# Kernel tuning notes

Measured on AMD Instinct MI355X. Metric: run time of the kernel, lower is better.

The kernel has to match this reference:

```python
import jax, jax.numpy as jnp
import numpy as np

L = 2          # num_blocks
E = 256        # embed_features
FIN = 64       # input_features
FF = 4 * E     # dim_feedforward
OUT = 10       # out_dim
WCTX = 64      # context_len
B, S = 2, 1024
LN_EPS = 1e-5


def _ln(x, g, b):
    m = jnp.mean(x, axis=-1, keepdims=True)
    v = jnp.mean((x - m) ** 2, axis=-1, keepdims=True)
    return (x - m) / jnp.sqrt(v + LN_EPS) * g + b


def setup_inputs() -> dict:
    key = jax.random.key(0)
    ks = jax.random.split(key, 12)
    s = 0.02
    return {
        "inputs": jax.random.normal(ks[0], (B, S, FIN), jnp.float32),
        "embed_w": jax.random.normal(ks[1], (E, FIN), jnp.float32) * s,
        "embed_b": jnp.zeros((E,), jnp.float32),
        "qkv_w": jax.random.normal(ks[2], (L, 3 * E, E), jnp.float32) * s,
        "qkv_b": jnp.zeros((L, 3 * E), jnp.float32),
        "attn_out_w": jax.random.normal(ks[3], (L, E, E), jnp.float32) * s,
        "attn_out_b": jnp.zeros((L, E), jnp.float32),
        "ln1_g": jnp.ones((L, E), jnp.float32),
        "ln1_b": jnp.zeros((L, E), jnp.float32),
        "ffn1_w": jax.random.normal(ks[4], (L, FF, E), jnp.float32) * s,
        "ffn1_b": jnp.zeros((L, FF), jnp.float32),
        "ffn2_w": jax.random.normal(ks[5], (L, E, FF), jnp.float32) * s,
        "ffn2_b": jnp.zeros((L, E), jnp.float32),
        "ln2_g": jnp.ones((L, E), jnp.float32),
        "ln2_b": jnp.zeros((L, E), jnp.float32),
        "head_w": jax.random.normal(ks[6], (OUT, E), jnp.float32) * s,
        "head_b": jnp.zeros((OUT,), jnp.float32),
        "context_len": WCTX,
    }


def reference(inputs, embed_w, embed_b, qkv_w, qkv_b, attn_out_w, attn_out_b,
              ln1_g, ln1_b, ffn1_w, ffn1_b, ffn2_w, ffn2_b, ln2_g, ln2_b,
              head_w, head_b, context_len):
    b, s, _ = inputs.shape
    e = embed_w.shape[0]
    nh = max(1, e // 64) * 2           # torch: nhead = max(1, E//64)*2
    hd = e // nh
    scale = 1.0 / np.sqrt(hd)
    w = context_len

    emb = inputs @ embed_w.T + embed_b                       # [B,S,E]
    # left-pad with W-1 zeros so window pos p = padded[p:p+W] (zeros for early pos)
    padded = jnp.pad(emb, ((0, 0), (w - 1, 0), (0, 0)))
    idx = jnp.arange(s)[:, None] + jnp.arange(w)[None, :]    # [S,W]
    x = padded[:, idx].reshape(b * s, w, e)                  # [B*S,W,E]

    nlayers = qkv_w.shape[0]
    for l in range(nlayers):
        qkv = x @ qkv_w[l].T + qkv_b[l]                      # [N,W,3E]
        q, k, v = jnp.split(qkv, 3, axis=-1)
        q = q.reshape(-1, w, nh, hd)
        k = k.reshape(-1, w, nh, hd)
        v = v.reshape(-1, w, nh, hd)
        scores = jnp.einsum('nqhd,nkhd->nhqk', q, k) * scale
        attn = jax.nn.softmax(scores, axis=-1)
        o = jnp.einsum('nhqk,nkhd->nqhd', attn, v).reshape(-1, w, e)
        o = o @ attn_out_w[l].T + attn_out_b[l]
        x = _ln(x + o, ln1_g[l], ln1_b[l])                   # post-norm (torch default)
        ff = jax.nn.silu(x @ ffn1_w[l].T + ffn1_b[l]) @ ffn2_w[l].T + ffn2_b[l]
        x = _ln(x + ff, ln2_g[l], ln2_b[l])

    out = x[:, -1, :] @ head_w.T + head_b                    # last token of each window
    return out.reshape(b, s, -1)
```

## Files before the change

kernel.cpp:

```cpp
#include <hip/hip_runtime.h>
#include <hip/hip_bf16.h>

#define BB_ 2
#define SS_ 1024
#define FIN_ 64
#define EE_ 256
#define FF_ 1024
#define NH_ 8
#define HD_ 32
#define OUT_ 10
#define NWIN (BB_ * SS_)
#define NT 512
#define SCALE_ 0.17677669529663687f
#define XBP 264
#define TPAD 1088

typedef unsigned short u16;
typedef unsigned int u32;
typedef __attribute__((ext_vector_type(8))) short bf8_t;
typedef __attribute__((ext_vector_type(4))) float f4_t;
#define MFMA_B16(a, b, c) __builtin_amdgcn_mfma_f32_16x16x32_bf16(a, b, c, 0, 0, 0)

__device__ __forceinline__ u16 bf16r(float f) {
    u32 u = __builtin_bit_cast(u32, f);
    return (u16)((u + 0x7FFFu + ((u >> 16) & 1u)) >> 16);
}
__device__ __forceinline__ u32 pk_bf16(float a, float b) {
    return (u32)bf16r(a) | ((u32)bf16r(b) << 16);
}
__device__ __forceinline__ float b2f(u16 h) {
    return __builtin_bit_cast(float, ((u32)h) << 16);
}
__device__ __forceinline__ float b2f_lo(u32 u) {
    return __builtin_bit_cast(float, u << 16);
}
__device__ __forceinline__ float b2f_hi(u32 u) {
    return __builtin_bit_cast(float, u & 0xFFFF0000u);
}

__device__ __forceinline__ float dot4(float4 a, float4 b) {
    return a.x * b.x + a.y * b.y + a.z * b.z + a.w * b.w;
}
__device__ __forceinline__ float wsum(float v) {
#pragma unroll
    for (int o = 32; o > 0; o >>= 1) v += __shfl_xor(v, o, 64);
    return v;
}
__device__ __forceinline__ float wmax(float v) {
#pragma unroll
    for (int o = 32; o > 0; o >>= 1) v = fmaxf(v, __shfl_xor(v, o, 64));
    return v;
}
__device__ __forceinline__ float silu_f(float h) { return h / (1.f + __expf(-h)); }

struct CvtArgs {
    const float* s[9];
    u16* d[9];
    int n[9];
};

__global__ void k_pre(const float* __restrict__ in, const float* __restrict__ embw,
                      const float* __restrict__ embb, const float* __restrict__ qkv_b,
                      CvtArgs ca, float* __restrict__ emb, u16* __restrict__ qkvp) {
    __shared__ float row[FIN_];
    const int blk = blockIdx.x;
    const int tid = threadIdx.x;
    if (blk < 2048) {
        if (tid < FIN_) row[tid] = in[blk * FIN_ + tid];
        __syncthreads();
        const float4* w4 = (const float4*)(embw + tid * FIN_);
        const float4* r4 = (const float4*)row;
        float s = 0.f;
#pragma unroll
        for (int c = 0; c < FIN_ / 4; ++c) s += dot4(w4[c], r4[c]);
        emb[blk * EE_ + tid] = s + embb[tid];
    } else if (blk < 2816) {
        const int b2 = blk - 2048;
#pragma unroll 1
        for (int seg = 0; seg < 9; ++seg) {
            const float* __restrict__ src = ca.s[seg];
            u16* __restrict__ dst = ca.d[seg];
            const int nn = ca.n[seg];
            for (int i = b2 * 256 + tid; i < nn; i += 768 * 256)
                dst[i] = bf16r(src[i]);
        }
    } else {
        const int b3 = blk - 2816;
        for (int f = b3 * 256 + tid; f < 2 * 64 * 768; f += 8 * 256) {
            const int bat = f / 49152;
            const int rem = f - bat * 49152;
            const int r = rem / 768, cl = rem - r * 768;
            qkvp[((size_t)bat * TPAD + r) * 768 + cl] = bf16r(qkv_b[cl]);
        }
    }
}

__global__ __launch_bounds__(512) void k_qkv0m(const float* __restrict__ emb,
                                               const u16* __restrict__ wq0b,
                                               const float* __restrict__ qkvb,
                                               u16* __restrict__ qkvp) {
    __shared__ u16 ab[16 * XBP];
    const int b = blockIdx.x;
    const int tid = threadIdx.x, lane = tid & 63, wv = tid >> 6;
    const int col = lane & 15, quad = lane >> 4;
    for (int idx = tid; idx < 16 * 256; idx += 512) {
        const int i = idx >> 8, e = idx & 255;
        ab[i * XBP + e] = bf16r(emb[(b * 16 + i) * EE_ + e]);
    }
    __syncthreads();
    f4_t acc[6];
#pragma unroll
    for (int nt = 0; nt < 6; ++nt) acc[nt] = (f4_t){0.f, 0.f, 0.f, 0.f};
#pragma unroll
    for (int ks = 0; ks < 8; ++ks) {
        const bf8_t ax = *(const bf8_t*)(ab + col * XBP + ks * 32 + quad * 8);
#pragma unroll
        for (int nt = 0; nt < 6; ++nt) {
            const int r = wv * 96 + nt * 16 + col;
            const bf8_t bw = *(const bf8_t*)(wq0b + r * EE_ + ks * 32 + quad * 8);
            acc[nt] = MFMA_B16(ax, bw, acc[nt]);
        }
    }
#pragma unroll
    for (int nt = 0; nt < 6; ++nt) {
        const int cc = wv * 96 + nt * 16 + col;
        const float bs = qkvb[cc];
#pragma unroll
        for (int j = 0; j < 4; ++j) {
            const int tok = b * 16 + quad * 4 + j;
            const int bb = tok >> 10;
            const size_t ti = (size_t)bb * TPAD + (tok & 1023) + 64;
            qkvp[ti * 768 + cc] = bf16r(acc[nt][j] + bs);
        }
    }
}

struct __align__(16) SMem {
    union {
        struct { u16 qkpb[9216]; u16 vt[4608]; } att;
        u16 hb[64 * 136];
        struct { u16 k1[64 * 66]; u16 v1[64 * 66]; } kv;
        struct { float red[64 * 17]; float stat[128]; } ln;
    } r1;
    u16 obxb[64 * XBP];
    float x1row[256];
    float o1b[256];
    float q1b[64];
    float sbuf2[128];
};

__device__ __forceinline__ void reg_ln(float (&x)[2][4][4], float* red, float* stat,
                                       u16* xb,
                                       float gc0, float gc1, float bc0, float bc1,
                                       int tid, int wv, int col, int quad,
                                       int colg0, int colg1) {
    float ps[4][4], pq[4][4];
#pragma unroll
    for (int mt = 0; mt < 4; ++mt)
#pragma unroll
        for (int j = 0; j < 4; ++j) {
            const float v0 = x[0][mt][j], v1 = x[1][mt][j];
            ps[mt][j] = v0 + v1;
            pq[mt][j] = v0 * v0 + v1 * v1;
        }
#pragma unroll
    for (int o = 1; o < 16; o <<= 1) {
#pragma unroll
        for (int mt = 0; mt < 4; ++mt)
#pragma unroll
            for (int j = 0; j < 4; ++j) {
                ps[mt][j] += __shfl_xor(ps[mt][j], o);
                pq[mt][j] += __shfl_xor(pq[mt][j], o);
            }
    }
    if (col == 0) {
#pragma unroll
        for (int mt = 0; mt < 4; ++mt)
#pragma unroll
            for (int j = 0; j < 4; ++j) {
                const int row = mt * 16 + quad * 4 + j;
                red[row * 17 + wv * 2] = ps[mt][j];
                red[row * 17 + wv * 2 + 1] = pq[mt][j];
            }
    }
    __syncthreads();
    if (tid < 64) {
        float s = 0.f, q = 0.f;
#pragma unroll
        for (int w = 0; w < 8; ++w) {
            s += red[tid * 17 + w * 2];
            q += red[tid * 17 + w * 2 + 1];
        }
        const float m = s * 0.00390625f;
        const float var = q * 0.00390625f - m * m;
        stat[tid * 2] = m;
        stat[tid * 2 + 1] = rsqrtf(var + 1e-5f);
    }
    __syncthreads();
#pragma unroll
    for (int mt = 0; mt < 4; ++mt)
#pragma unroll
        for (int j = 0; j < 4; ++j) {
            const int row = mt * 16 + quad * 4 + j;
            const float m = stat[row * 2];
            const float rs = stat[row * 2 + 1];
            const float xn0 = (x[0][mt][j] - m) * rs * gc0 + bc0;
            const float xn1 = (x[1][mt][j] - m) * rs * gc1 + bc1;
            x[0][mt][j] = xn0;
            x[1][mt][j] = xn1;
            const u32 w = pk_bf16(xn0, xn1);
            xb[row * XBP + colg0] = (u16)w;
            xb[row * XBP + colg1] = (u16)(w >> 16);
        }
}

__global__ __launch_bounds__(NT, 4) void k_fused(
    const float* __restrict__ emb, const u16* __restrict__ qkvp,
    const u16* __restrict__ w1b, const u16* __restrict__ w2b,
    const u16* __restrict__ wob, const u16* __restrict__ wkvb,
    const u16* __restrict__ wq1b, const u16* __restrict__ wob1,
    const float* __restrict__ qkv_b, const float* __restrict__ aob,
    const float* __restrict__ ln1g, const float* __restrict__ ln1b,
    const float* __restrict__ f1b, const float* __restrict__ f2b,
    const float* __restrict__ ln2g, const float* __restrict__ ln2b,
    float* __restrict__ x2g) {
    __shared__ SMem sm;
    const int n = blockIdx.x;
    const int bb = n >> 10, p = n & 1023;
    const int tid = threadIdx.x;
    const int lane = tid & 63, wv = tid >> 6;
    const int col = lane & 15, quad = lane >> 4;
    const int colg0 = wv * 32 + col, colg1 = colg0 + 16;

    const float* qkv_b1 = qkv_b + 3 * EE_;
    const float* aob1p = aob + EE_;

    const float aob_0 = aob[colg0], aob_1 = aob[colg1];
    const float f2b_0 = f2b[colg0], f2b_1 = f2b[colg1];
    const float g1_0 = ln1g[colg0], g1_1 = ln1g[colg1];
    const float b1_0 = ln1b[colg0], b1_1 = ln1b[colg1];
    const float g2_0 = ln2g[colg0], g2_1 = ln2g[colg1];
    const float b2_0 = ln2b[colg0], b2_1 = ln2b[colg1];

    for (int hp = 0; hp < 4; ++hp) {
        {
            const int i = tid >> 3, dg = tid & 7;
            const size_t rb = ((size_t)bb * TPAD + (p + 1 + i)) * 768 + hp * 64 + dg * 8;
            const uint4 q4 = *(const uint4*)(qkvp + rb);
            const uint4 k4 = *(const uint4*)(qkvp + rb + 256);
            const uint4 v4 = *(const uint4*)(qkvp + rb + 512);
            *(uint4*)(sm.r1.att.qkpb + i * 72 + dg * 8) = q4;
            *(uint4*)(sm.r1.att.qkpb + 4608 + i * 72 + dg * 8) = k4;
            union { uint4 u; u16 h[8]; } vu; vu.u = v4;
#pragma unroll
            for (int c = 0; c < 8; ++c)
                sm.r1.att.vt[(dg * 8 + c) * 72 + i] = vu.h[c];
        }
        __syncthreads();
        const int hh = wv >> 2, mt_ = wv & 3;
        const int r0 = mt_ * 16 + quad * 4;
        const bf8_t aq = *(const bf8_t*)(sm.r1.att.qkpb + (mt_ * 16 + col) * 72 + hh * 32 + quad * 8);
        f4_t sc[4];
#pragma unroll
        for (int nt = 0; nt < 4; ++nt) {
            const bf8_t bk = *(const bf8_t*)(sm.r1.att.qkpb + 4608 + (nt * 16 + col) * 72 + hh * 32 + quad * 8);
            f4_t z = {0.f, 0.f, 0.f, 0.f};
            sc[nt] = MFMA_B16(aq, bk, z);
        }
#pragma unroll
        for (int j = 0; j < 4; ++j) {
            float s0 = sc[0][j] * SCALE_, s1 = sc[1][j] * SCALE_;
            float s2v = sc[2][j] * SCALE_, s3 = sc[3][j] * SCALE_;
            float m = fmaxf(fmaxf(s0, s1), fmaxf(s2v, s3));
            m = fmaxf(m, __shfl_xor(m, 1)); m = fmaxf(m, __shfl_xor(m, 2));
            m = fmaxf(m, __shfl_xor(m, 4)); m = fmaxf(m, __shfl_xor(m, 8));
            const float e0 = __expf(s0 - m), e1 = __expf(s1 - m);
            const float e2 = __expf(s2v - m), e3 = __expf(s3 - m);
            float s = e0 + e1 + e2 + e3;
            s += __shfl_xor(s, 1); s += __shfl_xor(s, 2);
            s += __shfl_xor(s, 4); s += __shfl_xor(s, 8);
            const float inv = 1.f / s;
            sc[0][j] = e0 * inv; sc[1][j] = e1 * inv;
            sc[2][j] = e2 * inv; sc[3][j] = e3 * inv;
        }
        __syncthreads();
        u16* pbh = sm.r1.att.qkpb + hh * 4608;
#pragma unroll
        for (int nt = 0; nt < 4; ++nt) {
            const u32 w01 = pk_bf16(sc[nt][0], sc[nt][1]);
            const u32 w23 = pk_bf16(sc[nt][2], sc[nt][3]);
            u16* pp = pbh + r0 * 72 + nt * 16 + col;
            pp[0] = (u16)w01; pp[72] = (u16)(w01 >> 16);
            pp[144] = (u16)w23; pp[216] = (u16)(w23 >> 16);
        }
        f4_t ov[2];
        ov[0] = (f4_t){0.f, 0.f, 0.f, 0.f}; ov[1] = (f4_t){0.f, 0.f, 0.f, 0.f};
#pragma unroll
        for (int ks = 0; ks < 2; ++ks) {
            const bf8_t ap = *(const bf8_t*)(pbh + (mt_ * 16 + col) * 72 + ks * 32 + quad * 8);
#pragma unroll
            for (int ntl = 0; ntl < 2; ++ntl) {
                const bf8_t bv = *(const bf8_t*)(sm.r1.att.vt +
                                                 (hh * 32 + ntl * 16 + col) * 72 + ks * 32 + quad * 8);
                ov[ntl] = MFMA_B16(ap, bv, ov[ntl]);
            }
        }
#pragma unroll
        for (int ntl = 0; ntl < 2; ++ntl) {
            const u32 w01 = pk_bf16(ov[ntl][0], ov[ntl][1]);
            const u32 w23 = pk_bf16(ov[ntl][2], ov[ntl][3]);
            u16* oo = sm.obxb + r0 * XBP + (hp * 2 + hh) * 32 + ntl * 16 + col;
            oo[0] = (u16)w01; oo[XBP] = (u16)(w01 >> 16);
            oo[2 * XBP] = (u16)w23; oo[3 * XBP] = (u16)(w23 >> 16);
        }
        __syncthreads();
    }

    f4_t pacc[2][4];
#pragma unroll
    for (int a = 0; a < 2; ++a)
#pragma unroll
        for (int m = 0; m < 4; ++m) pacc[a][m] = (f4_t){0.f, 0.f, 0.f, 0.f};
#pragma unroll 2
    for (int ks = 0; ks < 8; ++ks) {
        bf8_t ao[4];
#pragma unroll
        for (int mt = 0; mt < 4; ++mt)
            ao[mt] = *(const bf8_t*)(sm.obxb + (mt * 16 + col) * XBP + ks * 32 + quad * 8);
#pragma unroll
        for (int ntl = 0; ntl < 2; ++ntl) {
            const bf8_t bw = *(const bf8_t*)(wob + ((wv * 2 + ntl) * 16 + col) * EE_ +
                                             ks * 32 + quad * 8);
#pragma unroll
            for (int mt = 0; mt < 4; ++mt) pacc[ntl][mt] = MFMA_B16(ao[mt], bw, pacc[ntl][mt]);
        }
    }

    float x[2][4][4];
#pragma unroll
    for (int mt = 0; mt < 4; ++mt)
#pragma unroll
        for (int j = 0; j < 4; ++j) {
            const int row = mt * 16 + quad * 4 + j;
            const int t = p - 63 + row;
            const size_t base = (size_t)((bb << 10) + t) * EE_;
            const float e0 = (t >= 0) ? emb[base + colg0] : 0.f;
            const float e1 = (t >= 0) ? emb[base + colg1] : 0.f;
            x[0][mt][j] = e0 + aob_0 + pacc[0][mt][j];
            x[1][mt][j] = e1 + aob_1 + pacc[1][mt][j];
        }
    __syncthreads();
    reg_ln(x, sm.r1.ln.red, sm.r1.ln.stat, sm.obxb,
           g1_0, g1_1, b1_0, b1_1, tid, wv, col, quad, colg0, colg1);
    __syncthreads();

    f4_t facc[2][4];
#pragma unroll
    for (int a = 0; a < 2; ++a)
#pragma unroll
        for (int m = 0; m < 4; ++m) facc[a][m] = (f4_t){0.f, 0.f, 0.f, 0.f};

    for (int c = 0; c < 8; ++c) {
        {
            f4_t hacc[4];
#pragma unroll
            for (int m = 0; m < 4; ++m) hacc[m] = (f4_t){0.f, 0.f, 0.f, 0.f};
            const int f = c * 128 + wv * 16 + col;
#pragma unroll 2
            for (int ks = 0; ks < 8; ++ks) {
                const bf8_t bw = *(const bf8_t*)(w1b + f * EE_ + ks * 32 + quad * 8);
#pragma unroll
                for (int mt = 0; mt < 4; ++mt) {
                    const bf8_t axr = *(const bf8_t*)(sm.obxb + (mt * 16 + col) * XBP + ks * 32 + quad * 8);
                    hacc[mt] = MFMA_B16(axr, bw, hacc[mt]);
                }
            }
            const float bv = f1b[f];
            const int lc = wv * 16 + col;
#pragma unroll
            for (int mt = 0; mt < 4; ++mt) {
                const u32 w01 = pk_bf16(silu_f(hacc[mt][0] + bv), silu_f(hacc[mt][1] + bv));
                const u32 w23 = pk_bf16(silu_f(hacc[mt][2] + bv), silu_f(hacc[mt][3] + bv));
                u16* hh2 = sm.r1.hb + (mt * 16 + quad * 4) * 136 + lc;
                hh2[0] = (u16)w01; hh2[136] = (u16)(w01 >> 16);
                hh2[272] = (u16)w23; hh2[408] = (u16)(w23 >> 16);
            }
        }
        __syncthreads();
        {
#pragma unroll 2
            for (int ks = 0; ks < 4; ++ks) {
                bf8_t ah[4];
#pragma unroll
                for (int mt = 0; mt < 4; ++mt)
                    ah[mt] = *(const bf8_t*)(sm.r1.hb + (mt * 16 + col) * 136 + ks * 32 + quad * 8);
#pragma unroll
                for (int ntl = 0; ntl < 2; ++ntl) {
                    const int e = (wv * 2 + ntl) * 16 + col;
                    const bf8_t bw = *(const bf8_t*)(w2b + e * FF_ + c * 128 + ks * 32 + quad * 8);
#pragma unroll
                    for (int mt = 0; mt < 4; ++mt) facc[ntl][mt] = MFMA_B16(ah[mt], bw, facc[ntl][mt]);
                }
            }
        }
        __syncthreads();
    }
#pragma unroll
    for (int mt = 0; mt < 4; ++mt)
#pragma unroll
        for (int j = 0; j < 4; ++j) {
            const int row = mt * 16 + quad * 4 + j;
            x[0][mt][j] = b2f(sm.obxb[row * XBP + colg0]) + facc[0][mt][j] + f2b_0;
            x[1][mt][j] = b2f(sm.obxb[row * XBP + colg1]) + facc[1][mt][j] + f2b_1;
        }
    __syncthreads();
    reg_ln(x, sm.r1.ln.red, sm.r1.ln.stat, sm.obxb,
           g2_0, g2_1, b2_0, b2_1, tid, wv, col, quad, colg0, colg1);
    if (quad == 3) {
        sm.x1row[colg0] = x[0][3][3];
        sm.x1row[colg1] = x[1][3][3];
    }
    __syncthreads();

    for (int hp = 0; hp < 4; ++hp) {
        {
            const int hf = wv >> 2, mtk = wv & 3;
            f4_t kacc[4];
#pragma unroll
            for (int a = 0; a < 4; ++a) kacc[a] = (f4_t){0.f, 0.f, 0.f, 0.f};
#pragma unroll 2
            for (int ks = 0; ks < 8; ++ks) {
                const bf8_t ax = *(const bf8_t*)(sm.obxb + (mtk * 16 + col) * XBP + ks * 32 + quad * 8);
#pragma unroll
                for (int nt = 0; nt < 4; ++nt) {
                    const int wr = hf * EE_ + hp * 64 + nt * 16 + col;
                    const bf8_t bw = *(const bf8_t*)(wkvb + wr * EE_ + ks * 32 + quad * 8);
                    kacc[nt] = MFMA_B16(ax, bw, kacc[nt]);
                }
            }
            u16* dst = hf ? sm.r1.kv.v1 : sm.r1.kv.k1;
#pragma unroll
            for (int nt = 0; nt < 4; ++nt) {
                const int cc = nt * 16 + col;
                const float bs = qkv_b1[(hf + 1) * EE_ + hp * 64 + cc];
                const u32 w01 = pk_bf16(kacc[nt][0] + bs, kacc[nt][1] + bs);
                const u32 w23 = pk_bf16(kacc[nt][2] + bs, kacc[nt][3] + bs);
                u16* dd = dst + (mtk * 16 + quad * 4) * 66 + cc;
                dd[0] = (u16)w01; dd[66] = (u16)(w01 >> 16);
                dd[132] = (u16)w23; dd[198] = (u16)(w23 >> 16);
            }
        }
        if (tid < 64) {
            const u16* wq = wq1b + (hp * 64 + tid) * EE_;
            float s = 0.f;
#pragma unroll 8
            for (int k2 = 0; k2 < 128; ++k2) {
                const u32 u = *(const u32*)(wq + k2 * 2);
                s += sm.x1row[2 * k2] * b2f_lo(u) + sm.x1row[2 * k2 + 1] * b2f_hi(u);
            }
            sm.q1b[tid] = s + qkv_b1[hp * 64 + tid];
        }
        __syncthreads();
        if (tid < 128) {
            const int hh = tid >> 6, jj = tid & 63;
            const u16* kr = sm.r1.kv.k1 + jj * 66 + hh * 32;
            const float* qv = sm.q1b + hh * 32;
            float s = 0.f;
#pragma unroll
            for (int d = 0; d < 32; ++d) s += qv[d] * b2f(kr[d]);
            s *= SCALE_;
            const float m = wmax(s);
            const float e = __expf(s - m);
            const float su = wsum(e);
            sm.sbuf2[tid] = e / su;
        }
        __syncthreads();
        if (tid < 64) {
            const int hh = tid >> 5, d = tid & 31;
            float acc = 0.f;
            for (int j = 0; j < 64; ++j)
                acc += sm.sbuf2[hh * 64 + j] * b2f(sm.r1.kv.v1[j * 66 + hh * 32 + d]);
            sm.o1b[hp * 64 + hh * 32 + d] = acc;
        }
        __syncthreads();
    }

    if (tid < 256) {
        const u16* wr = wob1 + tid * EE_;
        float s = 0.f;
#pragma unroll 8
        for (int k2 = 0; k2 < 128; ++k2) {
            const u32 u = *(const u32*)(wr + k2 * 2);
            s += sm.o1b[2 * k2] * b2f_lo(u) + sm.o1b[2 * k2 + 1] * b2f_hi(u);
        }
        x2g[n * EE_ + tid] = sm.x1row[tid] + s + aob1p[tid];
    }
}

__global__ __launch_bounds__(256) void k_tail(
    const float* __restrict__ x2g, const u16* __restrict__ w1b1,
    const float* __restrict__ f1b1, const u16* __restrict__ w2b1,
    const float* __restrict__ f2b1, const float* __restrict__ g1,
    const float* __restrict__ b1, const float* __restrict__ g2,
    const float* __restrict__ b2, const float* __restrict__ hw,
    const float* __restrict__ hbb, float* __restrict__ out) {
    __shared__ float xa[4 * 260];
    __shared__ float hid[4 * 1024];
    const int tid = threadIdx.x, lane = tid & 63, w = tid >> 6;
    const int n0 = blockIdx.x * 4;
    {
        const float* src = x2g + (size_t)(n0 + w) * EE_;
        const float v0 = src[lane], v1 = src[lane + 64], v2 = src[lane + 128], v3 = src[lane + 192];
        const float m = wsum(v0 + v1 + v2 + v3) * 0.00390625f;
        const float d0 = v0 - m, d1 = v1 - m, d2 = v2 - m, d3 = v3 - m;
        const float var = wsum(d0 * d0 + d1 * d1 + d2 * d2 + d3 * d3) * 0.00390625f;
        const float rs = rsqrtf(var + 1e-5f);
        xa[w * 260 + lane] = d0 * rs * g1[lane] + b1[lane];
        xa[w * 260 + lane + 64] = d1 * rs * g1[lane + 64] + b1[lane + 64];
        xa[w * 260 + lane + 128] = d2 * rs * g1[lane + 128] + b1[lane + 128];
        xa[w * 260 + lane + 192] = d3 * rs * g1[lane + 192] + b1[lane + 192];
    }
    __syncthreads();
#pragma unroll 1
    for (int r = 0; r < 4; ++r) {
        const int f = r * 256 + tid;
        const u16* wrow = w1b1 + f * EE_;
        float a0 = 0.f, a1 = 0.f, a2 = 0.f, a3 = 0.f;
#pragma unroll 4
        for (int k2 = 0; k2 < 128; ++k2) {
            const u32 u = *(const u32*)(wrow + k2 * 2);
            const float lo = b2f_lo(u), hi = b2f_hi(u);
            const float2 h0 = *(const float2*)(xa + 0 * 260 + k2 * 2);
            const float2 h1 = *(const float2*)(xa + 1 * 260 + k2 * 2);
            const float2 h2 = *(const float2*)(xa + 2 * 260 + k2 * 2);
            const float2 h3 = *(const float2*)(xa + 3 * 260 + k2 * 2);
            a0 += h0.x * lo + h0.y * hi;
            a1 += h1.x * lo + h1.y * hi;
            a2 += h2.x * lo + h2.y * hi;
            a3 += h3.x * lo + h3.y * hi;
        }
        const float bv = f1b1[f];
        hid[0 * 1024 + f] = silu_f(a0 + bv);
        hid[1 * 1024 + f] = silu_f(a1 + bv);
        hid[2 * 1024 + f] = silu_f(a2 + bv);
        hid[3 * 1024 + f] = silu_f(a3 + bv);
    }
    __syncthreads();
    {
        const u16* wrow = w2b1 + tid * FF_;
        float a0 = 0.f, a1 = 0.f, a2 = 0.f, a3 = 0.f;
#pragma unroll 4
        for (int k2 = 0; k2 < 512; ++k2) {
            const u32 u = *(const u32*)(wrow + k2 * 2);
            const float lo = b2f_lo(u), hi = b2f_hi(u);
            const float2 h0 = *(const float2*)(hid + 0 * 1024 + k2 * 2);
            const float2 h1 = *(const float2*)(hid + 1 * 1024 + k2 * 2);
            const float2 h2 = *(const float2*)(hid + 2 * 1024 + k2 * 2);
            const float2 h3 = *(const float2*)(hid + 3 * 1024 + k2 * 2);
            a0 += h0.x * lo + h0.y * hi;
            a1 += h1.x * lo + h1.y * hi;
            a2 += h2.x * lo + h2.y * hi;
            a3 += h3.x * lo + h3.y * hi;
        }
        const float bv = f2b1[tid];
        const float r0 = xa[0 * 260 + tid] + a0 + bv;
        const float r1 = xa[1 * 260 + tid] + a1 + bv;
        const float r2 = xa[2 * 260 + tid] + a2 + bv;
        const float r3 = xa[3 * 260 + tid] + a3 + bv;
        __syncthreads();
        xa[0 * 260 + tid] = r0;
        xa[1 * 260 + tid] = r1;
        xa[2 * 260 + tid] = r2;
        xa[3 * 260 + tid] = r3;
    }
    __syncthreads();
    {
        float* row = xa + w * 260;
        const float v0 = row[lane], v1 = row[lane + 64], v2 = row[lane + 128], v3 = row[lane + 192];
        const float m = wsum(v0 + v1 + v2 + v3) * 0.00390625f;
        const float d0 = v0 - m, d1 = v1 - m, d2 = v2 - m, d3 = v3 - m;
        const float var = wsum(d0 * d0 + d1 * d1 + d2 * d2 + d3 * d3) * 0.00390625f;
        const float rs = rsqrtf(var + 1e-5f);
        __syncthreads();
        row[lane] = d0 * rs * g2[lane] + b2[lane];
        row[lane + 64] = d1 * rs * g2[lane + 64] + b2[lane + 64];
        row[lane + 128] = d2 * rs * g2[lane + 128] + b2[lane + 128];
        row[lane + 192] = d3 * rs * g2[lane + 192] + b2[lane + 192];
    }
    __syncthreads();
    if (tid < 4 * OUT_) {
        const int win = tid / OUT_, o = tid % OUT_;
        const float* wr = hw + o * EE_;
        const float* xr = xa + win * 260;
        float s = 0.f;
#pragma unroll 8
        for (int c4 = 0; c4 < 64; ++c4)
            s += dot4(*(const float4*)(xr + c4 * 4), *(const float4*)(wr + c4 * 4));
        out[(n0 + win) * OUT_ + o] = s + hbb[o];
    }
}

extern "C" void kernel_launch(void* const* d_in, const int* in_sizes, int n_in,
                              void* d_out, int out_size, void* d_ws, size_t ws_size,
                              hipStream_t stream) {
    (void)in_sizes; (void)n_in; (void)out_size; (void)ws_size;
    const float* inputs = (const float*)d_in[0];
    const float* embed_w = (const float*)d_in[1];
    const float* embed_b = (const float*)d_in[2];
    const float* qkv_w = (const float*)d_in[3];
    const float* qkv_b = (const float*)d_in[4];
    const float* attn_out_w = (const float*)d_in[5];
    const float* attn_out_b = (const float*)d_in[6];
    const float* ln1_g = (const float*)d_in[7];
    const float* ln1_b = (const float*)d_in[8];
    const float* ffn1_w = (const float*)d_in[9];
    const float* ffn1_b = (const float*)d_in[10];
    const float* ffn2_w = (const float*)d_in[11];
    const float* ffn2_b = (const float*)d_in[12];
    const float* ln2_g = (const float*)d_in[13];
    const float* ln2_b = (const float*)d_in[14];
    const float* head_w = (const float*)d_in[15];
    const float* head_b = (const float*)d_in[16];
    float* out = (float*)d_out;

    char* wsb = (char*)d_ws;
    size_t off = 0;
    auto alloc = [&](size_t bytes) { char* pp = wsb + off; off += (bytes + 511) & ~511ull; return pp; };
    float* emb   = (float*)alloc((size_t)NWIN * EE_ * 4);
    u16*   qkvp  = (u16*)alloc((size_t)BB_ * TPAD * 768 * 2);
    float* x2g   = (float*)alloc((size_t)NWIN * EE_ * 4);
    u16*   w1b   = (u16*)alloc(FF_ * EE_ * 2);
    u16*   w2b   = (u16*)alloc(EE_ * FF_ * 2);
    u16*   wob   = (u16*)alloc(EE_ * EE_ * 2);
    u16*   wkvb  = (u16*)alloc(2 * EE_ * EE_ * 2);
    u16*   w1b1  = (u16*)alloc(FF_ * EE_ * 2);
    u16*   w2b1  = (u16*)alloc(EE_ * FF_ * 2);
    u16*   wob1  = (u16*)alloc(EE_ * EE_ * 2);
    u16*   wq1b  = (u16*)alloc(EE_ * EE_ * 2);
    u16*   wq0b  = (u16*)alloc(3 * EE_ * EE_ * 2);

    CvtArgs ca;
    ca.s[0] = ffn1_w;                            ca.d[0] = w1b;  ca.n[0] = FF_ * EE_;
    ca.s[1] = ffn2_w;                            ca.d[1] = w2b;  ca.n[1] = EE_ * FF_;
    ca.s[2] = attn_out_w;                        ca.d[2] = wob;  ca.n[2] = EE_ * EE_;
    ca.s[3] = qkv_w + 3 * EE_ * EE_ + EE_ * EE_; ca.d[3] = wkvb; ca.n[3] = 2 * EE_ * EE_;
    ca.s[4] = ffn1_w + FF_ * EE_;                ca.d[4] = w1b1; ca.n[4] = FF_ * EE_;
    ca.s[5] = ffn2_w + EE_ * FF_;                ca.d[5] = w2b1; ca.n[5] = EE_ * FF_;
    ca.s[6] = attn_out_w + EE_ * EE_;            ca.d[6] = wob1; ca.n[6] = EE_ * EE_;
    ca.s[7] = qkv_w + 3 * EE_ * EE_;             ca.d[7] = wq1b; ca.n[7] = EE_ * EE_;
    ca.s[8] = qkv_w;                             ca.d[8] = wq0b; ca.n[8] = 3 * EE_ * EE_;

    k_pre<<<2824, 256, 0, stream>>>(inputs, embed_w, embed_b, qkv_b, ca, emb, qkvp);
    k_qkv0m<<<NWIN / 16, 512, 0, stream>>>(emb, wq0b, qkv_b, qkvp);
    k_fused<<<NWIN, NT, 0, stream>>>(emb, qkvp, w1b, w2b, wob, wkvb,
                                     wq1b, wob1, qkv_b, attn_out_b,
                                     ln1_g, ln1_b, ffn1_b, ffn2_b,
                                     ln2_g, ln2_b, x2g);
    k_tail<<<NWIN / 4, 256, 0, stream>>>(x2g, w1b1, ffn1_b + FF_, w2b1, ffn2_b + EE_,
                                         ln1_g + EE_, ln1_b + EE_, ln2_g + EE_, ln2_b + EE_,
                                         head_w, head_b, out);
}
```

Baseline: 950.4 us.

## Split fused window kernel into attention and MLP kernels via global buffer

Splits the single per-window fused kernel into two kernels: k_attn runs layer-0 attention, the output projection and LN1, then writes the normalized bf16 window activations to a new global buffer. k_mlp reloads them and runs the FFN, LN2 and layer-1 last-token attention. The aim is to shrink each kernel's register and LDS footprint so more blocks fit per CU. In exchange it adds a 64x256 bf16 global round-trip per window (about 64 MB of traffic in total) and an extra kernel launch.

```diff
diff --git a/kernel.cpp b/kernel.cpp
--- a/kernel.cpp
+++ b/kernel.cpp
@@ -135,20 +135,6 @@
     }
 }
 
-struct __align__(16) SMem {
-    union {
-        struct { u16 qkpb[9216]; u16 vt[4608]; } att;
-        u16 hb[64 * 136];
-        struct { u16 k1[64 * 66]; u16 v1[64 * 66]; } kv;
-        struct { float red[64 * 17]; float stat[128]; } ln;
-    } r1;
-    u16 obxb[64 * XBP];
-    float x1row[256];
-    float o1b[256];
-    float q1b[64];
-    float sbuf2[128];
-};
-
 __device__ __forceinline__ void reg_ln(float (&x)[2][4][4], float* red, float* stat,
                                        u16* xb,
                                        float gc0, float gc1, float bc0, float bc1,
@@ -214,33 +200,26 @@
         }
 }
 
-__global__ __launch_bounds__(NT, 4) void k_fused(
+struct __align__(16) SMemA {
+    union {
+        struct { u16 qkpb[9216]; u16 vt[4608]; } att;
+        struct { float red[64 * 17]; float stat[128]; } ln;
+    } r1;
+    u16 obxb[64 * XBP];
+};
+
+__global__ __launch_bounds__(NT, 4) void k_attn(
     const float* __restrict__ emb, const u16* __restrict__ qkvp,
-    const u16* __restrict__ w1b, const u16* __restrict__ w2b,
-    const u16* __restrict__ wob, const u16* __restrict__ wkvb,
-    const u16* __restrict__ wq1b, const u16* __restrict__ wob1,
-    const float* __restrict__ qkv_b, const float* __restrict__ aob,
+    const u16* __restrict__ wob, const float* __restrict__ aob,
     const float* __restrict__ ln1g, const float* __restrict__ ln1b,
-    const float* __restrict__ f1b, const float* __restrict__ f2b,
-    const float* __restrict__ ln2g, const float* __restrict__ ln2b,
-    float* __restrict__ x2g) {
-    __shared__ SMem sm;
+    u16* __restrict__ xbg) {
+    __shared__ SMemA sm;
     const int n = blockIdx.x;
     const int bb = n >> 10, p = n & 1023;
     const int tid = threadIdx.x;
     const int lane = tid & 63, wv = tid >> 6;
     const int col = lane & 15, quad = lane >> 4;
     const int colg0 = wv * 32 + col, colg1 = colg0 + 16;
-
-    const float* qkv_b1 = qkv_b + 3 * EE_;
-    const float* aob1p = aob + EE_;
-
-    const float aob_0 = aob[colg0], aob_1 = aob[colg1];
-    const float f2b_0 = f2b[colg0], f2b_1 = f2b[colg1];
-    const float g1_0 = ln1g[colg0], g1_1 = ln1g[colg1];
-    const float b1_0 = ln1b[colg0], b1_1 = ln1b[colg1];
-    const float g2_0 = ln2g[colg0], g2_1 = ln2g[colg1];
-    const float b2_0 = ln2b[colg0], b2_1 = ln2b[colg1];
 
     for (int hp = 0; hp < 4; ++hp) {
         {
@@ -336,6 +315,7 @@
         }
     }
 
+    const float aob_0 = aob[colg0], aob_1 = aob[colg1];
     float x[2][4][4];
 #pragma unroll
     for (int mt = 0; mt < 4; ++mt)
@@ -351,7 +331,57 @@
         }
     __syncthreads();
     reg_ln(x, sm.r1.ln.red, sm.r1.ln.stat, sm.obxb,
-           g1_0, g1_1, b1_0, b1_1, tid, wv, col, quad, colg0, colg1);
+           ln1g[colg0], ln1g[colg1], ln1b[colg0], ln1b[colg1],
+           tid, wv, col, quad, colg0, colg1);
+    __syncthreads();
+    u16* dst = xbg + (size_t)n * 64 * 256;
+#pragma unroll
+    for (int k = 0; k < 4; ++k) {
+        const int idx = tid + k * NT;
+        const int row = idx >> 5, seg = idx & 31;
+        *(uint4*)(dst + row * 256 + seg * 8) = *(const uint4*)(sm.obxb + row * XBP + seg * 8);
+    }
+}
+
+struct __align__(16) SMemB {
+    u16 xb[64 * XBP];
+    union {
+        u16 hb[64 * 136];
+        struct { u16 k1[64 * 66]; u16 v1[64 * 66]; } kv;
+        struct { float red[64 * 17]; float stat[128]; } ln;
+    } c;
+    float x1row[256];
+    float o1b[256];
+    float q1b[64];
+    float sbuf2[128];
+};
+
+__global__ __launch_bounds__(NT, 4) void k_mlp(
+    const u16* __restrict__ xbg,
+    const u16* __restrict__ w1b, const u16* __restrict__ w2b,
+    const u16* __restrict__ wkvb, const u16* __restrict__ wq1b,
+    const u16* __restrict__ wob1,
+    const float* __restrict__ qkv_b, const float* __restrict__ aob,
+    const float* __restrict__ f1b, const float* __restrict__ f2b,
+    const float* __restrict__ ln2g, const float* __restrict__ ln2b,
+    float* __restrict__ x2g) {
+    __shared__ SMemB sm;
+    const int n = blockIdx.x;
+    const int tid = threadIdx.x;
+    const int lane = tid & 63, wv = tid >> 6;
+    const int col = lane & 15, quad = lane >> 4;
+    const int colg0 = wv * 32 + col, colg1 = colg0 + 16;
+
+    const float* qkv_b1 = qkv_b + 3 * EE_;
+    const float* aob1p = aob + EE_;
+
+    const u16* src = xbg + (size_t)n * 64 * 256;
+#pragma unroll
+    for (int k = 0; k < 4; ++k) {
+        const int idx = tid + k * NT;
+        const int row = idx >> 5, seg = idx & 31;
+        *(uint4*)(sm.xb + row * XBP + seg * 8) = *(const uint4*)(src + row * 256 + seg * 8);
+    }
     __syncthreads();
 
     f4_t facc[2][4];
@@ -371,7 +401,7 @@
                 const bf8_t bw = *(const bf8_t*)(w1b + f * EE_ + ks * 32 + quad * 8);
 #pragma unroll
                 for (int mt = 0; mt < 4; ++mt) {
-                    const bf8_t axr = *(const bf8_t*)(sm.obxb + (mt * 16 + col) * XBP + ks * 32 + quad * 8);
+                    const bf8_t axr = *(const bf8_t*)(sm.xb + (mt * 16 + col) * XBP + ks * 32 + quad * 8);
                     hacc[mt] = MFMA_B16(axr, bw, hacc[mt]);
                 }
             }
@@ -381,7 +411,7 @@
             for (int mt = 0; mt < 4; ++mt) {
                 const u32 w01 = pk_bf16(silu_f(hacc[mt][0] + bv), silu_f(hacc[mt][1] + bv));
                 const u32 w23 = pk_bf16(silu_f(hacc[mt][2] + bv), silu_f(hacc[mt][3] + bv));
-                u16* hh2 = sm.r1.hb + (mt * 16 + quad * 4) * 136 + lc;
+                u16* hh2 = sm.c.hb + (mt * 16 + quad * 4) * 136 + lc;
                 hh2[0] = (u16)w01; hh2[136] = (u16)(w01 >> 16);
                 hh2[272] = (u16)w23; hh2[408] = (u16)(w23 >> 16);
             }
@@ -393,7 +423,7 @@
                 bf8_t ah[4];
 #pragma unroll
                 for (int mt = 0; mt < 4; ++mt)
-                    ah[mt] = *(const bf8_t*)(sm.r1.hb + (mt * 16 + col) * 136 + ks * 32 + quad * 8);
+                    ah[mt] = *(const bf8_t*)(sm.c.hb + (mt * 16 + col) * 136 + ks * 32 + quad * 8);
 #pragma unroll
                 for (int ntl = 0; ntl < 2; ++ntl) {
                     const int e = (wv * 2 + ntl) * 16 + col;
@@ -405,17 +435,20 @@
         }
         __syncthreads();
     }
+    const float f2b_0 = f2b[colg0], f2b_1 = f2b[colg1];
+    float x[2][4][4];
 #pragma unroll
     for (int mt = 0; mt < 4; ++mt)
 #pragma unroll
         for (int j = 0; j < 4; ++j) {
             const int row = mt * 16 + quad * 4 + j;
-            x[0][mt][j] = b2f(sm.obxb[row * XBP + colg0]) + facc[0][mt][j] + f2b_0;
-            x[1][mt][j] = b2f(sm.obxb[row * XBP + colg1]) + facc[1][mt][j] + f2b_1;
-        }
-    __syncthreads();
-    reg_ln(x, sm.r1.ln.red, sm.r1.ln.stat, sm.obxb,
-           g2_0, g2_1, b2_0, b2_1, tid, wv, col, quad, colg0, colg1);
+            x[0][mt][j] = b2f(sm.xb[row * XBP + colg0]) + facc[0][mt][j] + f2b_0;
+            x[1][mt][j] = b2f(sm.xb[row * XBP + colg1]) + facc[1][mt][j] + f2b_1;
+        }
+    __syncthreads();
+    reg_ln(x, sm.c.ln.red, sm.c.ln.stat, sm.xb,
+           ln2g[colg0], ln2g[colg1], ln2b[colg0], ln2b[colg1],
+           tid, wv, col, quad, colg0, colg1);
     if (quad == 3) {
         sm.x1row[colg0] = x[0][3][3];
         sm.x1row[colg1] = x[1][3][3];
@@ -430,7 +463,7 @@
             for (int a = 0; a < 4; ++a) kacc[a] = (f4_t){0.f, 0.f, 0.f, 0.f};
 #pragma unroll 2
             for (int ks = 0; ks < 8; ++ks) {
-                const bf8_t ax = *(const bf8_t*)(sm.obxb + (mtk * 16 + col) * XBP + ks * 32 + quad * 8);
+                const bf8_t ax = *(const bf8_t*)(sm.xb + (mtk * 16 + col) * XBP + ks * 32 + quad * 8);
 #pragma unroll
                 for (int nt = 0; nt < 4; ++nt) {
                     const int wr = hf * EE_ + hp * 64 + nt * 16 + col;
@@ -438,7 +471,7 @@
                     kacc[nt] = MFMA_B16(ax, bw, kacc[nt]);
                 }
             }
-            u16* dst = hf ? sm.r1.kv.v1 : sm.r1.kv.k1;
+            u16* dst = hf ? sm.c.kv.v1 : sm.c.kv.k1;
 #pragma unroll
             for (int nt = 0; nt < 4; ++nt) {
                 const int cc = nt * 16 + col;
@@ -463,7 +496,7 @@
         __syncthreads();
         if (tid < 128) {
             const int hh = tid >> 6, jj = tid & 63;
-            const u16* kr = sm.r1.kv.k1 + jj * 66 + hh * 32;
+            const u16* kr = sm.c.kv.k1 + jj * 66 + hh * 32;
             const float* qv = sm.q1b + hh * 32;
             float s = 0.f;
 #pragma unroll
@@ -479,7 +512,7 @@
             const int hh = tid >> 5, d = tid & 31;
             float acc = 0.f;
             for (int j = 0; j < 64; ++j)
-                acc += sm.sbuf2[hh * 64 + j] * b2f(sm.r1.kv.v1[j * 66 + hh * 32 + d]);
+                acc += sm.sbuf2[hh * 64 + j] * b2f(sm.c.kv.v1[j * 66 + hh * 32 + d]);
             sm.o1b[hp * 64 + hh * 32 + d] = acc;
         }
         __syncthreads();
@@ -628,6 +661,7 @@
     auto alloc = [&](size_t bytes) { char* pp = wsb + off; off += (bytes + 511) & ~511ull; return pp; };
     float* emb   = (float*)alloc((size_t)NWIN * EE_ * 4);
     u16*   qkvp  = (u16*)alloc((size_t)BB_ * TPAD * 768 * 2);
+    u16*   xbg   = (u16*)alloc((size_t)NWIN * 64 * 256 * 2);
     float* x2g   = (float*)alloc((size_t)NWIN * EE_ * 4);
     u16*   w1b   = (u16*)alloc(FF_ * EE_ * 2);
     u16*   w2b   = (u16*)alloc(EE_ * FF_ * 2);
@@ -652,10 +686,10 @@
 
     k_pre<<<2824, 256, 0, stream>>>(inputs, embed_w, embed_b, qkv_b, ca, emb, qkvp);
     k_qkv0m<<<NWIN / 16, 512, 0, stream>>>(emb, wq0b, qkv_b, qkvp);
-    k_fused<<<NWIN, NT, 0, stream>>>(emb, qkvp, w1b, w2b, wob, wkvb,
-                                     wq1b, wob1, qkv_b, attn_out_b,
-                                     ln1_g, ln1_b, ffn1_b, ffn2_b,
-                                     ln2_g, ln2_b, x2g);
+    k_attn<<<NWIN, NT, 0, stream>>>(emb, qkvp, wob, attn_out_b, ln1_g, ln1_b, xbg);
+    k_mlp<<<NWIN, NT, 0, stream>>>(xbg, w1b, w2b, wkvb, wq1b, wob1,
+                                   qkv_b, attn_out_b, ffn1_b, ffn2_b,
+                                   ln2_g, ln2_b, x2g);
     k_tail<<<NWIN / 4, 256, 0, stream>>>(x2g, w1b1, ffn1_b + FF_, w2b1, ffn2_b + EE_,
                                          ln1_g + EE_, ln1_b + EE_, ln2_g + EE_, ln2_b + EE_,
                                          head_w, head_b, out);
```

Result: no change. 968.5 us (+1.9%).
